# Kernel tuning notes

Hardware: AMD Instinct MI355X
Metric: run time of the kernel (lower is better)

The kernel has to match this reference:

```python
import jax, jax.numpy as jnp
import numpy as np

DN = ('NCDHW', 'OIDHW', 'NCDHW')


def conv3d(x, w, stride=1):
    # kernel 3, SAME-style padding 1 (submanifold / strided sparse conv on a dense grid)
    return jax.lax.conv_general_dilated(
        x, w, window_strides=(stride,) * 3, padding=[(1, 1)] * 3,
        dimension_numbers=DN)


def tconv3d(x, w):
    # stride-2 transposed conv, kernel 3: doubles each spatial dim
    # (expressed as lhs-dilated conv; dilated = 2*in-1, pad (1,2) -> out = 2*in)
    return jax.lax.conv_general_dilated(
        x, w, window_strides=(1, 1, 1), padding=[(1, 2)] * 3,
        lhs_dilation=(2, 2, 2), dimension_numbers=DN)


def bn_relu(x, g, b, eps=1e-5):
    mu = jnp.mean(x, axis=(0, 2, 3, 4), keepdims=True)
    var = jnp.var(x, axis=(0, 2, 3, 4), keepdims=True)
    xh = (x - mu) * jax.lax.rsqrt(var + eps)
    c = (1, -1, 1, 1, 1)
    return jax.nn.relu(xh * g.reshape(c) + b.reshape(c))


def setup_inputs() -> dict:
    key = jax.random.key(0)
    ks = jax.random.split(key, 16)
    S = 0.1  # weight scale
    inp = {
        'x': jax.random.normal(ks[0], (1, 8, 128, 128, 128), jnp.float32),
        'w0': jax.random.normal(ks[1], (8, 8, 3, 3, 3), jnp.float32) * S,
        'g0': jnp.ones((8,), jnp.float32), 'b0': jnp.zeros((8,), jnp.float32),
        'w1': jax.random.normal(ks[2], (16, 8, 3, 3, 3), jnp.float32) * S,
        'g1': jnp.ones((16,), jnp.float32), 'b1': jnp.zeros((16,), jnp.float32),
        'w2': jax.random.normal(ks[3], (32, 16, 3, 3, 3), jnp.float32) * S,
        'g2': jnp.ones((32,), jnp.float32), 'b2': jnp.zeros((32,), jnp.float32),
        'w3': jax.random.normal(ks[4], (64, 32, 3, 3, 3), jnp.float32) * S,
        'g3': jnp.ones((64,), jnp.float32), 'b3': jnp.zeros((64,), jnp.float32),
        'wt3': jax.random.normal(ks[5], (32, 64, 3, 3, 3), jnp.float32) * S,
        'gt3': jnp.ones((32,), jnp.float32), 'bt3': jnp.zeros((32,), jnp.float32),
        'wt2': jax.random.normal(ks[6], (32, 64, 3, 3, 3), jnp.float32) * S,
        'gt2': jnp.ones((32,), jnp.float32), 'bt2': jnp.zeros((32,), jnp.float32),
        'wt1': jax.random.normal(ks[7], (24, 48, 3, 3, 3), jnp.float32) * S,
        'gt1': jnp.ones((24,), jnp.float32), 'bt1': jnp.zeros((24,), jnp.float32),
        'w_out': jax.random.normal(ks[8], (2, 32, 3, 3, 3), jnp.float32) * S,
    }
    return inp


def reference(x, w0, g0, b0, w1, g1, b1, w2, g2, b2, w3, g3, b3,
              wt3, gt3, bt3, wt2, gt2, bt2, wt1, gt1, bt1, w_out):
    # encoder
    s1 = bn_relu(conv3d(x, w0, 1), g0, b0)     # [1, 8,128^3]
    s2 = bn_relu(conv3d(s1, w1, 2), g1, b1)    # [1,16, 64^3]
    s4 = bn_relu(conv3d(s2, w2, 2), g2, b2)    # [1,32, 32^3]
    s8 = bn_relu(conv3d(s4, w3, 2), g3, b3)    # [1,64, 16^3]
    # decoder with skip concats
    d = bn_relu(tconv3d(s8, wt3), gt3, bt3)    # [1,32, 32^3]
    d = jnp.concatenate([d, s4], axis=1)       # [1,64, 32^3]
    d = bn_relu(tconv3d(d, wt2), gt2, bt2)     # [1,32, 64^3]
    d = jnp.concatenate([d, s2], axis=1)       # [1,48, 64^3]
    d = bn_relu(tconv3d(d, wt1), gt1, bt1)     # [1,24,128^3]
    d = jnp.concatenate([d, s1], axis=1)       # [1,32,128^3]
    return conv3d(d, w_out, 1)                 # [1, 2,128^3]
```

## Files before the change

kernel.cpp:

```cpp
#include <hip/hip_runtime.h>
#include <hip/hip_bf16.h>

typedef __hip_bfloat16 bf16;
#define TPB 256

typedef __attribute__((ext_vector_type(8))) short s8v;
typedef __attribute__((ext_vector_type(4))) float f4v;

__device__ inline void wred2(float& a, float& b) {
#pragma unroll
    for (int o = 32; o > 0; o >>= 1) {
        a += __shfl_down(a, o, 64);
        b += __shfl_down(b, o, 64);
    }
}

__device__ inline void bnco(const float* st, const float* g, const float* b,
                            float invN, int ch0, float* sc, float* sh) {
#pragma unroll
    for (int j = 0; j < 8; ++j) {
        int ch = ch0 + j;
        float mean = st[2 * ch] * invN;
        float var  = st[2 * ch + 1] * invN - mean * mean;
        sc[j] = rsqrtf(var + 1e-5f) * g[ch];
        sh[j] = b[ch] - mean * sc[j];
    }
}
__device__ inline void bnap(const uint4& u, const float* sc, const float* sh,
                            bf16* o) {
    const unsigned short* s = (const unsigned short*)&u;
#pragma unroll
    for (int j = 0; j < 8; ++j) {
        float v = __uint_as_float((unsigned)s[j] << 16);
        v = v * sc[j] + sh[j];
        o[j] = __float2bfloat16(v > 0.f ? v : 0.f);
    }
}

__global__ __launch_bounds__(TPB) void repack_wbc_k(
    const float* __restrict__ w, bf16* __restrict__ wb,
    int OCR, int IC, int KK, int NT)
{
    int idx = blockIdx.x * TPB + threadIdx.x;
    int tot = KK * NT * 512;
    if (idx >= tot) return;
    int j = idx & 7;
    int l = (idx >> 3) & 63;
    int rest = idx >> 9;
    int nt = rest % NT;
    int kk = rest / NT;
    int n = nt * 16 + (l & 15);
    int k = kk * 32 + (l >> 4) * 8 + j;
    int tap = k / IC, ci = k % IC;
    float v = (n < OCR && tap < 27) ? w[(n * IC + ci) * 27 + tap] : 0.f;
    wb[idx] = __float2bfloat16(v);
}

__global__ __launch_bounds__(TPB) void repack_wb_k(
    const float* __restrict__ w, bf16* __restrict__ wb,
    int OCR, int IC, int KC, int NT)
{
    int idx = blockIdx.x * TPB + threadIdx.x;
    int tot = 27 * KC * NT * 512;
    if (idx >= tot) return;
    int j = idx & 7;
    int l = (idx >> 3) & 63;
    int rest = idx >> 9;
    int nt = rest % NT;
    int kc = (rest / NT) % KC;
    int kt = rest / (NT * KC);
    int n = nt * 16 + (l & 15);
    int k = kc * 32 + (l >> 4) * 8 + j;
    float v = (n < OCR && k < IC) ? w[(n * IC + k) * 27 + kt] : 0.f;
    wb[idx] = __float2bfloat16(v);
}

__global__ __launch_bounds__(64) void repack_wc_k(
    const float* __restrict__ w, bf16* __restrict__ wc)
{
    int idx = blockIdx.x * 64 + threadIdx.x;
    if (idx >= 1728) return;
    int ci = idx & 31;
    int n = (idx >> 5) & 1;
    int tap = idx >> 6;
    wc[idx] = __float2bfloat16(w[(n * 32 + ci) * 27 + tap]);
}

__global__ __launch_bounds__(TPB) void sumcol_k(
    const float* __restrict__ p, int nrow, float* __restrict__ out)
{
    __shared__ float ws[4];
    const long col = blockIdx.x;
    float s = 0.f;
    for (int r = threadIdx.x; r < nrow; r += TPB) s += p[col * nrow + r];
    float d = 0.f;
    wred2(s, d);
    if ((threadIdx.x & 63) == 0) ws[threadIdx.x >> 6] = s;
    __syncthreads();
    if (threadIdx.x == 0) out[col] = ws[0] + ws[1] + ws[2] + ws[3];
}

template <int IC, int OCR, int STRIDE, int TZ, int TY, int TX,
          bool INF32, bool CFOUT, bool DOSTATS, bool BNIN>
__global__ __launch_bounds__(TPB) void conv_mfma_k(
    const void* __restrict__ in_, const bf16* __restrict__ wb,
    bf16* __restrict__ out, float* __restrict__ outf,
    int ID, int IH, int IW, int OD, int OH, int OW, int CSin, int CSout,
    float* __restrict__ prt, int nrow,
    const float* __restrict__ bst, const float* __restrict__ bg,
    const float* __restrict__ bb, float binvN)
{
    constexpr int EZ = STRIDE * TZ + 3 - STRIDE;
    constexpr int EY = STRIDE * TY + 3 - STRIDE;
    constexpr int EX = STRIDE * TX + 3 - STRIDE;
    constexpr int NR = EZ * EY * EX;
    constexpr int PITCH = (IC == 8) ? 8 : IC + 8;
    constexpr int CHK = IC / 8;
    constexpr int KK = (27 * IC + 31) / 32;
    constexpr int NT = (OCR + 15) / 16;
    constexpr int MT = (TY * TX) / 16;
    constexpr int MROWS = 16 / TX;
    static_assert(TZ == 4, "wave = z-slice");
    static_assert(TPB % CHK == 0, "thread-fixed chunk");
    __shared__ __align__(16) bf16 si[NR * PITCH];
    __shared__ float ps[4][2 * 16 * NT];
    const int ntx = OW / TX, nty = OH / TY;
    const int bx = blockIdx.x % ntx;
    const int by = (blockIdx.x / ntx) % nty;
    const int bz = blockIdx.x / (ntx * nty);
    const int x0 = bx * TX * STRIDE - 1;
    const int y0 = by * TY * STRIDE - 1;
    const int z0 = bz * TZ * STRIDE - 1;

    if constexpr (INF32) {
        static_assert(!INF32 || (IC == 8 && PITCH == 8), "INF32 assumes IC=8");
        const float* x = (const float*)in_;
        const long S = (long)ID * IH * IW;
        for (int i = threadIdx.x; i < NR; i += TPB) {
            int rx = i % EX; int t = i / EX; int ry = t % EY; int rz = t / EY;
            int gz = z0 + rz, gy = y0 + ry, gx = x0 + rx;
            bf16 o[8];
            if ((unsigned)gz < (unsigned)ID && (unsigned)gy < (unsigned)IH &&
                (unsigned)gx < (unsigned)IW) {
                const float* p = x + ((long)gz * IH + gy) * IW + gx;
#pragma unroll
                for (int c = 0; c < 8; ++c)
                    o[c] = __float2bfloat16(p[(long)c * S]);
            } else {
#pragma unroll
                for (int c = 0; c < 8; ++c) o[c] = __float2bfloat16(0.f);
            }
            *(uint4*)(si + i * 8) = *(const uint4*)o;
        }
    } else {
        const bf16* in = (const bf16*)in_;
        float sc[8], sh[8];
        if constexpr (BNIN)
            bnco(bst, bg, bb, binvN, (threadIdx.x % CHK) * 8, sc, sh);
        for (int i = threadIdx.x; i < NR * CHK; i += TPB) {
            int r = i / CHK, c = i % CHK;
            int rx = r % EX, ry = (r / EX) % EY, rz = r / (EX * EY);
            int gz = z0 + rz, gy = y0 + ry, gx = x0 + rx;
            bool ok = (unsigned)gz < (unsigned)ID && (unsigned)gy < (unsigned)IH &&
                      (unsigned)gx < (unsigned)IW;
            uint4 u = make_uint4(0u, 0u, 0u, 0u);
            if (ok)
                u = *(const uint4*)(in + (((long)gz * IH + gy) * IW + gx) * CSin + c * 8);
            if constexpr (BNIN) {
                bf16 o[8];
                if (ok) bnap(u, sc, sh, o);
                else {
#pragma unroll
                    for (int j = 0; j < 8; ++j) o[j] = __float2bfloat16(0.f);
                }
                *(uint4*)(si + r * PITCH + c * 8) = *(const uint4*)o;
            } else {
                *(uint4*)(si + r * PITCH + c * 8) = u;
            }
        }
    }
    __syncthreads();

    const int w = threadIdx.x >> 6;
    const int lane = threadIdx.x & 63;
    const int q = lane >> 4, m = lane & 15;
    const int vy = m / TX, vx = m % TX;

    f4v acc[MT][NT];
#pragma unroll
    for (int mt = 0; mt < MT; ++mt)
#pragma unroll
        for (int nt = 0; nt < NT; ++nt) acc[mt][nt] = (f4v)(0.f);

#define KBODY                                                                  \
    {                                                                          \
        int flat = kk * 32 + q * 8;                                            \
        int tb = flat / IC; if (tb > 26) tb = 26;                              \
        const int cb = flat % IC;                                              \
        const int kz = tb / 9, ky = (tb / 3) % 3, kx = tb % 3;                 \
        s8v bfr[NT];                                                           \
        _Pragma("unroll")                                                      \
        for (int nt = 0; nt < NT; ++nt)                                        \
            bfr[nt] = *(const s8v*)(wb + ((long)(kk * NT + nt) << 9) + lane * 8); \
        const int iz = w * STRIDE + kz;                                        \
        const int ixc = vx * STRIDE + kx;                                      \
        _Pragma("unroll")                                                      \
        for (int mt = 0; mt < MT; ++mt) {                                      \
            int iy = (mt * MROWS + vy) * STRIDE + ky;                          \
            int row = (iz * EY + iy) * EX + ixc;                               \
            s8v av = *(const s8v*)(si + row * PITCH + cb);                     \
            _Pragma("unroll")                                                  \
            for (int nt = 0; nt < NT; ++nt)                                    \
                acc[mt][nt] = __builtin_amdgcn_mfma_f32_16x16x32_bf16(         \
                    av, bfr[nt], acc[mt][nt], 0, 0, 0);                        \
        }                                                                      \
    }

    if constexpr (KK <= 7) {
#pragma unroll
        for (int kk = 0; kk < KK; ++kk) KBODY
    } else {
#pragma unroll 1
        for (int kk = 0; kk < KK; ++kk) KBODY
    }
#undef KBODY

    float ls[NT], ls2[NT];
#pragma unroll
    for (int nt = 0; nt < NT; ++nt) { ls[nt] = 0.f; ls2[nt] = 0.f; }
    const int oz = bz * TZ + w;
#pragma unroll
    for (int mt = 0; mt < MT; ++mt)
#pragma unroll
        for (int nt = 0; nt < NT; ++nt) {
            const int n_ch = nt * 16 + m;
            if constexpr (DOSTATS) {
#pragma unroll
                for (int r = 0; r < 4; ++r) {
                    float v = acc[mt][nt][r];
                    ls[nt] += v; ls2[nt] += v * v;
                }
            }
            if (n_ch < OCR) {
#pragma unroll
                for (int r = 0; r < 4; ++r) {
                    int vrow = 4 * q + r;
                    int oy = by * TY + mt * MROWS + vrow / TX;
                    int ox = bx * TX + vrow % TX;
                    long vox = ((long)oz * OH + oy) * OW + ox;
                    if constexpr (CFOUT) {
                        long Sout = (long)OD * OH * OW;
                        outf[(long)n_ch * Sout + vox] = acc[mt][nt][r];
                    } else {
                        out[vox * CSout + n_ch] = __float2bfloat16(acc[mt][nt][r]);
                    }
                }
            }
        }
    if constexpr (DOSTATS) {
#pragma unroll
        for (int nt = 0; nt < NT; ++nt) {
            float t = ls[nt], t2 = ls2[nt];
            t  += __shfl_down(t, 32, 64);  t  += __shfl_down(t, 16, 64);
            t2 += __shfl_down(t2, 32, 64); t2 += __shfl_down(t2, 16, 64);
            if (lane < 16) {
                ps[w][2 * (nt * 16 + lane)]     = t;
                ps[w][2 * (nt * 16 + lane) + 1] = t2;
            }
        }
        __syncthreads();
        if (threadIdx.x < 2 * OCR) {
            float v = ps[0][threadIdx.x] + ps[1][threadIdx.x]
                    + ps[2][threadIdx.x] + ps[3][threadIdx.x];
            prt[(long)threadIdx.x * nrow + blockIdx.x] = v;
        }
    }
}

__global__ __launch_bounds__(TPB, 4) void outconv_k(
    const bf16* __restrict__ cat, const bf16* __restrict__ s1v,
    const bf16* __restrict__ wc, float* __restrict__ outf,
    const float* __restrict__ stats, const float* __restrict__ g,
    const float* __restrict__ b,
    const float* __restrict__ stS, const float* __restrict__ gS,
    const float* __restrict__ bS, float invN)
{
    constexpr int EY = 10, EX = 10, PITCH = 32;
    __shared__ __align__(16) bf16 si[600 * PITCH];
    const int bx = blockIdx.x & 15;
    const int by = (blockIdx.x >> 4) & 15;
    const int bz = blockIdx.x >> 8;
    const int x0 = bx * 8 - 1, y0 = by * 8 - 1, z0 = bz * 4 - 1;

    const int c4 = threadIdx.x & 3;
    float sc[8], sh[8];
    if (c4 < 3) bnco(stats, g, b, invN, c4 * 8, sc, sh);
    else        bnco(stS, gS, bS, invN, 0, sc, sh);

    const int col = threadIdx.x >> 2;
    const bool inter = (bx > 0) & (bx < 15) & (by > 0) & (by < 15) &
                       (bz > 0) & (bz < 31);
#pragma unroll
    for (int cp = 0; cp < 2; ++cp) {
        const int cc = col + cp * 64;
        if (cc < 100) {
            const int ry = cc / 10, rx = cc - ry * 10;
            const int gy = y0 + ry, gx = x0 + rx;
            const long vyx = (long)gy * 128 + gx;
            uint4 u[6];
            if (inter) {
#pragma unroll
                for (int rz = 0; rz < 6; ++rz) {
                    long vox = ((long)(z0 + rz) << 14) + vyx;
                    const bf16* p = (c4 == 3) ? (s1v + vox * 8)
                                              : (cat + vox * 24 + c4 * 8);
                    u[rz] = *(const uint4*)p;
                }
#pragma unroll
                for (int rz = 0; rz < 6; ++rz) {
                    bf16 o[8];
                    bnap(u[rz], sc, sh, o);
                    *(uint4*)(si + (rz * 100 + cc) * PITCH + c4 * 8) =
                        *(const uint4*)o;
                }
            } else {
                const bool yxok = ((unsigned)gy < 128u) & ((unsigned)gx < 128u);
                unsigned zm = 0u;
#pragma unroll
                for (int rz = 0; rz < 6; ++rz) {
                    u[rz] = make_uint4(0u, 0u, 0u, 0u);
                    int gz = z0 + rz;
                    if (yxok && (unsigned)gz < 128u) {
                        long vox = ((long)gz << 14) + vyx;
                        const bf16* p = (c4 == 3) ? (s1v + vox * 8)
                                                  : (cat + vox * 24 + c4 * 8);
                        u[rz] = *(const uint4*)p;
                        zm |= 1u << rz;
                    }
                }
#pragma unroll
                for (int rz = 0; rz < 6; ++rz) {
                    bf16 o[8];
                    if ((zm >> rz) & 1u) bnap(u[rz], sc, sh, o);
                    else {
#pragma unroll
                        for (int j = 0; j < 8; ++j) o[j] = __float2bfloat16(0.f);
                    }
                    *(uint4*)(si + (rz * 100 + cc) * PITCH + c4 * 8) =
                        *(const uint4*)o;
                }
            }
        }
    }
    __syncthreads();

    const int w = threadIdx.x >> 6;
    const int lane = threadIdx.x & 63;
    const int q = lane >> 4, m = lane & 15;
    const int vy = (m >> 3) & 1, vx = m & 7;

    f4v acc[4];
#pragma unroll
    for (int mt = 0; mt < 4; ++mt) acc[mt] = (f4v)(0.f);

    const bf16* wcl = wc + (m & 1) * 32 + q * 8;
#pragma unroll
    for (int kz = 0; kz < 3; ++kz) {
#pragma unroll
        for (int kx = 0; kx < 3; ++kx) {
            const bf16* sp = si +
                ((((w + kz) * EY + vy) * EX) + vx + kx) * PITCH + q * 8;
            s8v a[9];
#pragma unroll
            for (int j = 0; j < 9; ++j)
                a[j] = *(const s8v*)(sp + j * (EX * PITCH));
            const bf16* bp = wcl + (kz * 9 + kx) * 64;
            s8v bf0 = *(const s8v*)(bp);
            s8v bf1 = *(const s8v*)(bp + 3 * 64);
            s8v bf2 = *(const s8v*)(bp + 6 * 64);
#pragma unroll
            for (int mt = 0; mt < 4; ++mt) {
                acc[mt] = __builtin_amdgcn_mfma_f32_16x16x32_bf16(
                    a[2 * mt + 0], bf0, acc[mt], 0, 0, 0);
                acc[mt] = __builtin_amdgcn_mfma_f32_16x16x32_bf16(
                    a[2 * mt + 1], bf1, acc[mt], 0, 0, 0);
                acc[mt] = __builtin_amdgcn_mfma_f32_16x16x32_bf16(
                    a[2 * mt + 2], bf2, acc[mt], 0, 0, 0);
            }
        }
    }
    if (m < 2) {
        const long Sout = 128L * 128 * 128;
        const int oz = bz * 4 + w;
#pragma unroll
        for (int mt = 0; mt < 4; ++mt) {
#pragma unroll
            for (int r = 0; r < 4; ++r) {
                int vrow = 4 * q + r;
                int oy = by * 8 + mt * 2 + (vrow >> 3);
                int ox = bx * 8 + (vrow & 7);
                outf[(long)m * Sout + (((long)oz * 128 + oy) * 128 + ox)] =
                    acc[mt][r];
            }
        }
    }
}

template <int IC, int OCR>
__global__ __launch_bounds__(TPB) void tconv_mfma_k(
    const bf16* __restrict__ in, const bf16* __restrict__ wb,
    bf16* __restrict__ out, int ID, int IH, int IW, int CSin, int CSout,
    float* __restrict__ prt, int nrow,
    const float* __restrict__ st0, const float* __restrict__ g0p,
    const float* __restrict__ b0p, const float* __restrict__ st1,
    const float* __restrict__ g1p, const float* __restrict__ b1p,
    float binvN, int C0)
{
    constexpr int KC = (IC + 31) / 32;
    constexpr int NT = (OCR + 15) / 16;
    constexpr int TZ = 4, TY = 4, TX = 8;
    constexpr int EZ = TZ + 1, EY = TY + 1, EX = TX + 1;
    constexpr int NR = EZ * EY * EX;
    constexpr int PITCH = (IC == 48) ? 64 : 72;
    constexpr int CHKS = 8;
    constexpr int CHK = IC / 8;
    __shared__ __align__(16) bf16 si[NR * PITCH];
    __shared__ float ps[4][64];
    const int ntx = IW / TX, nty = IH / TY;
    const int bx = blockIdx.x % ntx;
    const int by = (blockIdx.x / ntx) % nty;
    const int bz = blockIdx.x / (ntx * nty);
    const int x0 = bx * TX, y0 = by * TY, z0 = bz * TZ;

    {
        const int c = threadIdx.x & 7;
        float sc[8], sh[8];
#pragma unroll
        for (int j = 0; j < 8; ++j) { sc[j] = 1.f; sh[j] = 0.f; }
        if (c < CHK) {
#pragma unroll
            for (int j = 0; j < 8; ++j) {
                int ch = c * 8 + j;
                const float* st; const float* gg; const float* bbq; int k;
                if (ch < C0) { st = st0; gg = g0p; bbq = b0p; k = ch; }
                else         { st = st1; gg = g1p; bbq = b1p; k = ch - C0; }
                float mean = st[2 * k] * binvN;
                float var  = st[2 * k + 1] * binvN - mean * mean;
                sc[j] = rsqrtf(var + 1e-5f) * gg[k];
                sh[j] = bbq[k] - mean * sc[j];
            }
        }
        for (int i = threadIdx.x; i < NR * CHKS; i += TPB) {
            int r = i >> 3, cc = i & 7;
            int rx = r % EX, ry = (r / EX) % EY, rz = r / (EX * EY);
            int gz = z0 + rz, gy = y0 + ry, gx = x0 + rx;
            bool ok = (cc < CHK) && gz < ID && gy < IH && gx < IW;
            uint4 u = make_uint4(0u, 0u, 0u, 0u);
            if (ok)
                u = *(const uint4*)(in + (((long)gz * IH + gy) * IW + gx) * CSin + cc * 8);
            bf16 o[8];
            if (ok) bnap(u, sc, sh, o);
            else {
#pragma unroll
                for (int j = 0; j < 8; ++j) o[j] = __float2bfloat16(0.f);
            }
            *(uint4*)(si + r * PITCH + cc * 8) = *(const uint4*)o;
        }
    }
    __syncthreads();
    const int w = threadIdx.x >> 6;
    const int lane = threadIdx.x & 63;
    const int q = lane >> 4, m = lane & 15;
    const int vy = m >> 3, vx = m & 7;
    const int OH = 2 * IH, OW = 2 * IW;
    float ls[NT], ls2[NT];
#pragma unroll
    for (int nt = 0; nt < NT; ++nt) { ls[nt] = 0.f; ls2[nt] = 0.f; }

#pragma unroll 1
    for (int cls = 0; cls < 8; ++cls) {
        const int pz = (cls >> 2) & 1, py = (cls >> 1) & 1, px = cls & 1;
        const int ny = 1 + py, nx = 1 + px;
        const int ntap = (1 + pz) * ny * nx;
        f4v acc[2][NT];
#pragma unroll
        for (int mt = 0; mt < 2; ++mt)
#pragma unroll
            for (int nt = 0; nt < NT; ++nt) acc[mt][nt] = (f4v)(0.f);
#pragma unroll 1
        for (int s = 0; s < ntap; ++s) {
            int a = s / (ny * nx), b = (s / nx) % ny, cc = s % nx;
            int dz = pz ? a : 0, dy = py ? b : 0, dx = px ? cc : 0;
            int kz = pz ? (a ? 2 : 0) : 1;
            int ky = py ? (b ? 2 : 0) : 1;
            int kx = px ? (cc ? 2 : 0) : 1;
            int kt = kz * 9 + ky * 3 + kx;
#pragma unroll
            for (int kc = 0; kc < KC; ++kc) {
                const bf16* bp = wb + (long)((kt * KC + kc) * NT) * 512 + lane * 8;
                s8v b0 = *(const s8v*)bp;
                s8v b1 = *(const s8v*)(bp + 512);
#pragma unroll
                for (int mt = 0; mt < 2; ++mt) {
                    int row = ((w + dz) * EY + (2 * mt + vy + dy)) * EX + (vx + dx);
                    s8v av = *(const s8v*)(si + row * PITCH + kc * 32 + q * 8);
                    acc[mt][0] = __builtin_amdgcn_mfma_f32_16x16x32_bf16(
                        av, b0, acc[mt][0], 0, 0, 0);
                    acc[mt][1] = __builtin_amdgcn_mfma_f32_16x16x32_bf16(
                        av, b1, acc[mt][1], 0, 0, 0);
                }
            }
        }
        const int z = 2 * (z0 + w) + pz;
#pragma unroll
        for (int mt = 0; mt < 2; ++mt)
#pragma unroll
            for (int nt = 0; nt < NT; ++nt) {
                const int n_ch = nt * 16 + m;
#pragma unroll
                for (int r = 0; r < 4; ++r) {
                    float v = acc[mt][nt][r];
                    ls[nt] += v; ls2[nt] += v * v;
                }
                if (n_ch < OCR) {
#pragma unroll
                    for (int r = 0; r < 4; ++r) {
                        int vrow = 4 * q + r;
                        int yy = 2 * (y0 + 2 * mt + (vrow >> 3)) + py;
                        int xx = 2 * (x0 + (vrow & 7)) + px;
                        out[(((long)z * OH + yy) * OW + xx) * CSout + n_ch] =
                            __float2bfloat16(acc[mt][nt][r]);
                    }
                }
            }
    }
#pragma unroll
    for (int nt = 0; nt < NT; ++nt) {
        float t = ls[nt], t2 = ls2[nt];
        t  += __shfl_down(t, 32, 64);  t  += __shfl_down(t, 16, 64);
        t2 += __shfl_down(t2, 32, 64); t2 += __shfl_down(t2, 16, 64);
        if (lane < 16) {
            ps[w][2 * (nt * 16 + lane)]     = t;
            ps[w][2 * (nt * 16 + lane) + 1] = t2;
        }
    }
    __syncthreads();
    if (threadIdx.x < 2 * OCR) {
        float v = ps[0][threadIdx.x] + ps[1][threadIdx.x] + ps[2][threadIdx.x]
                + ps[3][threadIdx.x];
        prt[(long)threadIdx.x * nrow + blockIdx.x] = v;
    }
}

static inline int nblocks(long n, int per) { return (int)((n + per - 1) / per); }

extern "C" void kernel_launch(void* const* d_in, const int* in_sizes, int n_in,
                              void* d_out, int out_size, void* d_ws, size_t ws_size,
                              hipStream_t stream)
{
    const float* x    = (const float*)d_in[0];
    const float* w0   = (const float*)d_in[1];
    const float* g0   = (const float*)d_in[2];
    const float* b0   = (const float*)d_in[3];
    const float* w1   = (const float*)d_in[4];
    const float* g1   = (const float*)d_in[5];
    const float* b1   = (const float*)d_in[6];
    const float* w2   = (const float*)d_in[7];
    const float* g2   = (const float*)d_in[8];
    const float* b2   = (const float*)d_in[9];
    const float* w3   = (const float*)d_in[10];
    const float* g3   = (const float*)d_in[11];
    const float* b3   = (const float*)d_in[12];
    const float* wt3  = (const float*)d_in[13];
    const float* gt3  = (const float*)d_in[14];
    const float* bt3  = (const float*)d_in[15];
    const float* wt2  = (const float*)d_in[16];
    const float* gt2  = (const float*)d_in[17];
    const float* bt2  = (const float*)d_in[18];
    const float* wt1  = (const float*)d_in[19];
    const float* gt1  = (const float*)d_in[20];
    const float* bt1  = (const float*)d_in[21];
    const float* wout = (const float*)d_in[22];

    const long S128 = 128L * 128 * 128;
    const long S64  = 64L * 64 * 64;
    const long S32  = 32L * 32 * 32;
    const long S16  = 16L * 16 * 16;

    float* stats = (float*)d_ws;
    bf16*  wc    = (bf16*)((char*)d_ws + 2048);
    bf16* base = (bf16*)((char*)d_ws + 2048 + 27648);
    bf16* cat1 = base;
    bf16* cat2 = cat1 + S128 * 24;
    bf16* cat3 = cat2 + S64 * 48;
    bf16* s8   = cat3 + S32 * 64;
    bf16* s1   = s8 + S16 * 64;
    bf16* s2 = cat2 + 32;
    bf16* s4 = cat3 + 32;

    bf16*  wbb  = (bf16*)d_out;
    bf16*  wbt1 = wbb;
    bf16*  wbt2 = wbb + 55296;
    bf16*  wbt3 = wbb + 110592;
    bf16*  wb0  = wbb + 165888;
    bf16*  wb1  = wbb + 169472;
    bf16*  wb2  = wbb + 173056;
    bf16*  wb3  = wbb + 187392;
    float* prt  = (float*)d_out + 524288;

    repack_wb_k <<<nblocks(55296, TPB), TPB, 0, stream>>>(wt1, wbt1, 24, 48, 2, 2);
    repack_wb_k <<<nblocks(55296, TPB), TPB, 0, stream>>>(wt2, wbt2, 32, 64, 2, 2);
    repack_wb_k <<<nblocks(55296, TPB), TPB, 0, stream>>>(wt3, wbt3, 32, 64, 2, 2);
    repack_wbc_k<<<nblocks(3584,  TPB), TPB, 0, stream>>>(w0,  wb0,  8,  8,  7, 1);
    repack_wbc_k<<<nblocks(3584,  TPB), TPB, 0, stream>>>(w1,  wb1,  16, 8,  7, 1);
    repack_wbc_k<<<nblocks(14336, TPB), TPB, 0, stream>>>(w2,  wb2,  32, 16, 14, 2);
    repack_wbc_k<<<nblocks(55296, TPB), TPB, 0, stream>>>(w3,  wb3,  64, 32, 27, 4);
    repack_wc_k <<<27, 64, 0, stream>>>(wout, wc);

    conv_mfma_k<8, 8, 1, 4, 8, 8, true, false, true, false><<<8192, TPB, 0, stream>>>(
        x, wb0, s1, nullptr, 128, 128, 128, 128, 128, 128, 0, 8, prt, 8192,
        nullptr, nullptr, nullptr, 0.f);
    sumcol_k<<<16, TPB, 0, stream>>>(prt, 8192, stats + 0);

    conv_mfma_k<8, 16, 2, 4, 8, 8, false, false, true, true><<<1024, TPB, 0, stream>>>(
        s1, wb1, s2, nullptr, 128, 128, 128, 64, 64, 64, 8, 48, prt, 1024,
        stats + 0, g0, b0, 1.f / S128);
    sumcol_k<<<32, TPB, 0, stream>>>(prt, 1024, stats + 16);

    conv_mfma_k<16, 32, 2, 4, 4, 4, false, false, true, true><<<512, TPB, 0, stream>>>(
        s2, wb2, s4, nullptr, 64, 64, 64, 32, 32, 32, 48, 64, prt, 512,
        stats + 16, g1, b1, 1.f / S64);
    sumcol_k<<<64, TPB, 0, stream>>>(prt, 512, stats + 48);

    conv_mfma_k<32, 64, 2, 4, 4, 4, false, false, true, true><<<64, TPB, 0, stream>>>(
        s4, wb3, s8, nullptr, 32, 32, 32, 16, 16, 16, 64, 64, prt, 64,
        stats + 48, g2, b2, 1.f / S32);
    sumcol_k<<<128, TPB, 0, stream>>>(prt, 64, stats + 112);

    tconv_mfma_k<64, 32><<<32, TPB, 0, stream>>>(
        s8, wbt3, cat3, 16, 16, 16, 64, 64, prt, 32,
        stats + 112, g3, b3, stats + 112, g3, b3, 1.f / S16, 64);
    sumcol_k<<<64, TPB, 0, stream>>>(prt, 32, stats + 240);

    tconv_mfma_k<64, 32><<<256, TPB, 0, stream>>>(
        cat3, wbt2, cat2, 32, 32, 32, 64, 48, prt, 256,
        stats + 240, gt3, bt3, stats + 48, g2, b2, 1.f / S32, 32);
    sumcol_k<<<64, TPB, 0, stream>>>(prt, 256, stats + 304);

    tconv_mfma_k<48, 24><<<2048, TPB, 0, stream>>>(
        cat2, wbt1, cat1, 64, 64, 64, 48, 24, prt, 2048,
        stats + 304, gt2, bt2, stats + 16, g1, b1, 1.f / S64, 32);
    sumcol_k<<<48, TPB, 0, stream>>>(prt, 2048, stats + 368);

    outconv_k<<<8192, TPB, 0, stream>>>(
        cat1, s1, wc, (float*)d_out, stats + 368, gt1, bt1,
        stats + 0, g0, b0, 1.f / S128);
}
```

Baseline: 518.5 us.

## Merge weight repacks into one launch and accumulate BN stats with atomics

```diff
diff --git a/kernel.cpp b/kernel.cpp
--- a/kernel.cpp
+++ b/kernel.cpp
@@ -6,14 +6,6 @@
 
 typedef __attribute__((ext_vector_type(8))) short s8v;
 typedef __attribute__((ext_vector_type(4))) float f4v;
-
-__device__ inline void wred2(float& a, float& b) {
-#pragma unroll
-    for (int o = 32; o > 0; o >>= 1) {
-        a += __shfl_down(a, o, 64);
-        b += __shfl_down(b, o, 64);
-    }
-}
 
 __device__ inline void bnco(const float* st, const float* g, const float* b,
                             float invN, int ch0, float* sc, float* sh) {
@@ -37,11 +29,11 @@
     }
 }
 
-__global__ __launch_bounds__(TPB) void repack_wbc_k(
-    const float* __restrict__ w, bf16* __restrict__ wb,
-    int OCR, int IC, int KK, int NT)
-{
-    int idx = blockIdx.x * TPB + threadIdx.x;
+__device__ inline void rep_wbc(const float* __restrict__ w,
+                               bf16* __restrict__ wb,
+                               int OCR, int IC, int KK, int NT, int vb)
+{
+    int idx = vb * TPB + (int)threadIdx.x;
     int tot = KK * NT * 512;
     if (idx >= tot) return;
     int j = idx & 7;
@@ -56,11 +48,11 @@
     wb[idx] = __float2bfloat16(v);
 }
 
-__global__ __launch_bounds__(TPB) void repack_wb_k(
-    const float* __restrict__ w, bf16* __restrict__ wb,
-    int OCR, int IC, int KC, int NT)
-{
-    int idx = blockIdx.x * TPB + threadIdx.x;
+__device__ inline void rep_wb(const float* __restrict__ w,
+                              bf16* __restrict__ wb,
+                              int OCR, int IC, int KC, int NT, int vb)
+{
+    int idx = vb * TPB + (int)threadIdx.x;
     int tot = 27 * KC * NT * 512;
     if (idx >= tot) return;
     int j = idx & 7;
@@ -75,10 +67,10 @@
     wb[idx] = __float2bfloat16(v);
 }
 
-__global__ __launch_bounds__(64) void repack_wc_k(
-    const float* __restrict__ w, bf16* __restrict__ wc)
-{
-    int idx = blockIdx.x * 64 + threadIdx.x;
+__device__ inline void rep_wc(const float* __restrict__ w,
+                              bf16* __restrict__ wc, int vb)
+{
+    int idx = vb * TPB + (int)threadIdx.x;
     if (idx >= 1728) return;
     int ci = idx & 31;
     int n = (idx >> 5) & 1;
@@ -86,18 +78,29 @@
     wc[idx] = __float2bfloat16(w[(n * 32 + ci) * 27 + tap]);
 }
 
-__global__ __launch_bounds__(TPB) void sumcol_k(
-    const float* __restrict__ p, int nrow, float* __restrict__ out)
-{
-    __shared__ float ws[4];
-    const long col = blockIdx.x;
-    float s = 0.f;
-    for (int r = threadIdx.x; r < nrow; r += TPB) s += p[col * nrow + r];
-    float d = 0.f;
-    wred2(s, d);
-    if ((threadIdx.x & 63) == 0) ws[threadIdx.x >> 6] = s;
-    __syncthreads();
-    if (threadIdx.x == 0) out[col] = ws[0] + ws[1] + ws[2] + ws[3];
+__global__ __launch_bounds__(TPB) void init_all_k(
+    const float* wt1, const float* wt2, const float* wt3,
+    const float* w0, const float* w1, const float* w2, const float* w3,
+    const float* wout,
+    bf16* wbt1, bf16* wbt2, bf16* wbt3,
+    bf16* wb0, bf16* wb1, bf16* wb2, bf16* wb3, bf16* wc,
+    float* stats)
+{
+    int b = blockIdx.x;
+    if (b == 0) {
+        stats[threadIdx.x] = 0.f;
+        stats[threadIdx.x + 256] = 0.f;
+        return;
+    }
+    b -= 1;
+    if (b < 216) { rep_wb(wt1, wbt1, 24, 48, 2, 2, b); return; } b -= 216;
+    if (b < 216) { rep_wb(wt2, wbt2, 32, 64, 2, 2, b); return; } b -= 216;
+    if (b < 216) { rep_wb(wt3, wbt3, 32, 64, 2, 2, b); return; } b -= 216;
+    if (b < 14)  { rep_wbc(w0, wb0, 8,  8,  7,  1, b); return; } b -= 14;
+    if (b < 14)  { rep_wbc(w1, wb1, 16, 8,  7,  1, b); return; } b -= 14;
+    if (b < 56)  { rep_wbc(w2, wb2, 32, 16, 14, 2, b); return; } b -= 56;
+    if (b < 216) { rep_wbc(w3, wb3, 64, 32, 27, 4, b); return; } b -= 216;
+    rep_wc(wout, wc, b);
 }
 
 template <int IC, int OCR, int STRIDE, int TZ, int TY, int TX,
@@ -106,7 +109,7 @@
     const void* __restrict__ in_, const bf16* __restrict__ wb,
     bf16* __restrict__ out, float* __restrict__ outf,
     int ID, int IH, int IW, int OD, int OH, int OW, int CSin, int CSout,
-    float* __restrict__ prt, int nrow,
+    float* __restrict__ sdst,
     const float* __restrict__ bst, const float* __restrict__ bg,
     const float* __restrict__ bb, float binvN)
 {
@@ -272,7 +275,7 @@
         if (threadIdx.x < 2 * OCR) {
             float v = ps[0][threadIdx.x] + ps[1][threadIdx.x]
                     + ps[2][threadIdx.x] + ps[3][threadIdx.x];
-            prt[(long)threadIdx.x * nrow + blockIdx.x] = v;
+            atomicAdd(sdst + threadIdx.x, v);
         }
     }
 }
@@ -410,7 +413,7 @@
 __global__ __launch_bounds__(TPB) void tconv_mfma_k(
     const bf16* __restrict__ in, const bf16* __restrict__ wb,
     bf16* __restrict__ out, int ID, int IH, int IW, int CSin, int CSout,
-    float* __restrict__ prt, int nrow,
+    float* __restrict__ sdst,
     const float* __restrict__ st0, const float* __restrict__ g0p,
     const float* __restrict__ b0p, const float* __restrict__ st1,
     const float* __restrict__ g1p, const float* __restrict__ b1p,
@@ -548,11 +551,9 @@
     if (threadIdx.x < 2 * OCR) {
         float v = ps[0][threadIdx.x] + ps[1][threadIdx.x] + ps[2][threadIdx.x]
                 + ps[3][threadIdx.x];
-        prt[(long)threadIdx.x * nrow + blockIdx.x] = v;
-    }
-}
-
-static inline int nblocks(long n, int per) { return (int)((n + per - 1) / per); }
+        atomicAdd(sdst + threadIdx.x, v);
+    }
+}
 
 extern "C" void kernel_launch(void* const* d_in, const int* in_sizes, int n_in,
                               void* d_out, int out_size, void* d_ws, size_t ws_size,
@@ -606,51 +607,38 @@
     bf16*  wb1  = wbb + 169472;
     bf16*  wb2  = wbb + 173056;
     bf16*  wb3  = wbb + 187392;
-    float* prt  = (float*)d_out + 524288;
-
-    repack_wb_k <<<nblocks(55296, TPB), TPB, 0, stream>>>(wt1, wbt1, 24, 48, 2, 2);
-    repack_wb_k <<<nblocks(55296, TPB), TPB, 0, stream>>>(wt2, wbt2, 32, 64, 2, 2);
-    repack_wb_k <<<nblocks(55296, TPB), TPB, 0, stream>>>(wt3, wbt3, 32, 64, 2, 2);
-    repack_wbc_k<<<nblocks(3584,  TPB), TPB, 0, stream>>>(w0,  wb0,  8,  8,  7, 1);
-    repack_wbc_k<<<nblocks(3584,  TPB), TPB, 0, stream>>>(w1,  wb1,  16, 8,  7, 1);
-    repack_wbc_k<<<nblocks(14336, TPB), TPB, 0, stream>>>(w2,  wb2,  32, 16, 14, 2);
-    repack_wbc_k<<<nblocks(55296, TPB), TPB, 0, stream>>>(w3,  wb3,  64, 32, 27, 4);
-    repack_wc_k <<<27, 64, 0, stream>>>(wout, wc);
+
+    init_all_k<<<956, TPB, 0, stream>>>(
+        wt1, wt2, wt3, w0, w1, w2, w3, wout,
+        wbt1, wbt2, wbt3, wb0, wb1, wb2, wb3, wc, stats);
 
     conv_mfma_k<8, 8, 1, 4, 8, 8, true, false, true, false><<<8192, TPB, 0, stream>>>(
-        x, wb0, s1, nullptr, 128, 128, 128, 128, 128, 128, 0, 8, prt, 8192,
+        x, wb0, s1, nullptr, 128, 128, 128, 128, 128, 128, 0, 8, stats + 0,
         nullptr, nullptr, nullptr, 0.f);
-    sumcol_k<<<16, TPB, 0, stream>>>(prt, 8192, stats + 0);
 
     conv_mfma_k<8, 16, 2, 4, 8, 8, false, false, true, true><<<1024, TPB, 0, stream>>>(
-        s1, wb1, s2, nullptr, 128, 128, 128, 64, 64, 64, 8, 48, prt, 1024,
+        s1, wb1, s2, nullptr, 128, 128, 128, 64, 64, 64, 8, 48, stats + 16,
         stats + 0, g0, b0, 1.f / S128);
-    sumcol_k<<<32, TPB, 0, stream>>>(prt, 1024, stats + 16);
 
     conv_mfma_k<16, 32, 2, 4, 4, 4, false, false, true, true><<<512, TPB, 0, stream>>>(
-        s2, wb2, s4, nullptr, 64, 64, 64, 32, 32, 32, 48, 64, prt, 512,
+        s2, wb2, s4, nullptr, 64, 64, 64, 32, 32, 32, 48, 64, stats + 48,
         stats + 16, g1, b1, 1.f / S64);
-    sumcol_k<<<64, TPB, 0, stream>>>(prt, 512, stats + 48);
 
     conv_mfma_k<32, 64, 2, 4, 4, 4, false, false, true, true><<<64, TPB, 0, stream>>>(
-        s4, wb3, s8, nullptr, 32, 32, 32, 16, 16, 16, 64, 64, prt, 64,
+        s4, wb3, s8, nullptr, 32, 32, 32, 16, 16, 16, 64, 64, stats + 112,
         stats + 48, g2, b2, 1.f / S32);
-    sumcol_k<<<128, TPB, 0, stream>>>(prt, 64, stats + 112);
 
     tconv_mfma_k<64, 32><<<32, TPB, 0, stream>>>(
-        s8, wbt3, cat3, 16, 16, 16, 64, 64, prt, 32,
+        s8, wbt3, cat3, 16, 16, 16, 64, 64, stats + 240,
         stats + 112, g3, b3, stats + 112, g3, b3, 1.f / S16, 64);
-    sumcol_k<<<64, TPB, 0, stream>>>(prt, 32, stats + 240);
 
     tconv_mfma_k<64, 32><<<256, TPB, 0, stream>>>(
-        cat3, wbt2, cat2, 32, 32, 32, 64, 48, prt, 256,
+        cat3, wbt2, cat2, 32, 32, 32, 64, 48, stats + 304,
         stats + 240, gt3, bt3, stats + 48, g2, b2, 1.f / S32, 32);
-    sumcol_k<<<64, TPB, 0, stream>>>(prt, 256, stats + 304);
 
     tconv_mfma_k<48, 24><<<2048, TPB, 0, stream>>>(
-        cat2, wbt1, cat1, 64, 64, 64, 48, 24, prt, 2048,
+        cat2, wbt1, cat1, 64, 64, 64, 48, 24, stats + 368,
         stats + 304, gt2, bt2, stats + 16, g1, b1, 1.f / S64, 32);
-    sumcol_k<<<48, TPB, 0, stream>>>(prt, 2048, stats + 368);
 
     outconv_k<<<8192, TPB, 0, stream>>>(
         cat1, s1, wc, (float*)d_out, stats + 368, gt1, bt1,
```

Result: slower. 587.6 us (+13.3%).
